# Kernel optimization log

Hardware: AMD Instinct MI355X
Metric: run time of the kernel (lower is better)

Reference implementation:

```python
import jax, jax.numpy as jnp
import numpy as np

B = 1048576
S = 8
K = 10  # n_facts
EPS = 1e-8
ENTROPY_W = 0.01
DIVERSITY_W = 0.1


def setup_inputs() -> dict:
    key = jax.random.key(0)
    k1, k2, k3, k4, k5 = jax.random.split(key, 5)
    p = jax.random.uniform(k1, (B, 2, K), dtype=jnp.float32) + 1e-3
    pCS = p / jnp.sum(p, axis=-1, keepdims=True)  # normalized probs like Categorical
    base_loss = jax.random.uniform(k2, (1,), dtype=jnp.float32)
    Y = jax.random.randint(k3, (B,), 0, 19, dtype=jnp.int32)
    samples1 = jax.random.randint(k4, (S, B), 0, K, dtype=jnp.int32)
    samples2 = jax.random.randint(k5, (S, B), 0, K, dtype=jnp.int32)
    return {"pCS": pCS, "base_loss": base_loss, "Y": Y,
            "samples1": samples1, "samples2": samples2}


def reference(pCS, base_loss, Y, samples1, samples2):
    n_facts = pCS.shape[-1]
    s = samples1.shape[0]
    p1 = pCS[:, 0, :]  # [B, K]
    p2 = pCS[:, 1, :]
    # entropy regularization
    ent1 = -jnp.sum(p1 * jnp.log(p1 + EPS), axis=-1).mean()
    ent2 = -jnp.sum(p2 * jnp.log(p2 + EPS), axis=-1).mean()
    entropy_loss = -(ent1 + ent2) / 2
    # diversity: count unique (d1,d2) pairs per batch element (vectorized bincount-style)
    pairs = (samples1 * n_facts + samples2).T  # [B, S]
    eq = pairs[:, :, None] == pairs[:, None, :]  # [B, S, S]
    earlier = jnp.tril(jnp.ones((s, s), dtype=bool), k=-1)  # j < i
    dup = jnp.any(eq & earlier[None], axis=-1)  # [B, S] True if seen before
    unique_counts = jnp.sum(~dup, axis=-1).astype(jnp.float32)  # [B]
    diversity = unique_counts.mean()
    max_diversity = min(s, n_facts * n_facts)
    diversity_ratio = diversity / max_diversity
    diversity_loss = -jnp.log(diversity_ratio + EPS)
    # REINFORCE leave-one-out (computed, not added to total in original)
    pred_labels = samples1 + samples2  # [S, B] (addition task)
    correct = (pred_labels == Y[None, :]).astype(jnp.float32)
    sample_acc = correct.mean()
    b_idx = jnp.arange(p1.shape[0])[None, :]
    log_probs = jnp.log(p1)[b_idx, samples1] + jnp.log(p2)[b_idx, samples2]  # [S, B]
    baseline = (jnp.sum(correct, axis=0, keepdims=True) - correct) / (s - 1 + EPS)
    advantage = jax.lax.stop_gradient(correct - baseline)
    rloo_loss = -jnp.mean(log_probs * advantage)
    total_loss = base_loss[0] + ENTROPY_W * entropy_loss + DIVERSITY_W * diversity_loss
    return jnp.stack([total_loss, rloo_loss, diversity_loss, sample_acc])
```

## Files before the change

kernel.cpp:

```cpp
#include <hip/hip_runtime.h>

#define S_CONST 8
#define K_CONST 10
#define EPSF 1e-8f

__global__ __launch_bounds__(256) void fml_reduce(
        const float* __restrict__ pCS,
        const int* __restrict__ Y,
        const int* __restrict__ s1g,
        const int* __restrict__ s2g,
        double* __restrict__ partials,
        int B)
{
    __shared__ float sp[4][64 * 20];
    __shared__ float red[4][4];

    const int lane = threadIdx.x & 63;
    const int wv   = threadIdx.x >> 6;
    float* sw = sp[wv];

    float ent = 0.f, uniq = 0.f, corr = 0.f, rloo = 0.f;

    const int nchunks = (B + 63) >> 6;
    const int gwaves  = gridDim.x << 2;
    for (int ch = (blockIdx.x << 2) + wv; ch < nchunks; ch += gwaves) {
        const int base = ch << 6;
        const int row  = base + lane;
        const bool full = (base + 64) <= B;
        const bool inb  = full || (row < B);

        int y = 0;
        int a1[S_CONST], a2[S_CONST];
        if (inb) {
            y = Y[row];
            #pragma unroll
            for (int s = 0; s < S_CONST; ++s) {
                a1[s] = s1g[(size_t)s * B + row];
                a2[s] = s2g[(size_t)s * B + row];
            }
        } else {
            y = -1;
            #pragma unroll
            for (int s = 0; s < S_CONST; ++s) { a1[s] = 0; a2[s] = 0; }
        }

        const float4* src = reinterpret_cast<const float4*>(pCS + (size_t)base * 20);
        float4* dst = reinterpret_cast<float4*>(sw);
        #pragma unroll
        for (int k = 0; k < 5; ++k) {
            const int g = lane + (k << 6);
            float4 v = make_float4(1.f, 1.f, 1.f, 1.f);
            if (full || (base + g / 5) < B) v = src[g];
            ent += v.x * __logf(v.x) + v.y * __logf(v.y)
                 + v.z * __logf(v.z) + v.w * __logf(v.w);
            dst[g] = v;
        }
        __builtin_amdgcn_wave_barrier();

        if (inb) {
            int pr[S_CONST];
            float c[S_CONST];
            float csum = 0.f;
            #pragma unroll
            for (int s = 0; s < S_CONST; ++s) {
                pr[s] = a1[s] * K_CONST + a2[s];
                c[s]  = (a1[s] + a2[s] == y) ? 1.f : 0.f;
                csum += c[s];
            }
            corr += csum;

            #pragma unroll
            for (int i = 0; i < S_CONST; ++i) {
                bool dup = false;
                #pragma unroll
                for (int j = 0; j < i; ++j) dup = dup || (pr[i] == pr[j]);
                uniq += dup ? 0.f : 1.f;
            }

            const float* my = &sw[lane * 20];
            #pragma unroll
            for (int s = 0; s < S_CONST; ++s) {
                const float g1 = my[a1[s]];
                const float g2 = my[10 + a2[s]];
                const float adv = c[s] - (csum - c[s]) / 7.0f;
                rloo += __logf(g1 * g2) * adv;
            }
        }
        __builtin_amdgcn_wave_barrier();
    }

    #pragma unroll
    for (int off = 32; off >= 1; off >>= 1) {
        ent  += __shfl_xor(ent,  off);
        uniq += __shfl_xor(uniq, off);
        corr += __shfl_xor(corr, off);
        rloo += __shfl_xor(rloo, off);
    }

    if (lane == 0) {
        red[wv][0] = ent; red[wv][1] = uniq;
        red[wv][2] = corr; red[wv][3] = rloo;
    }
    __syncthreads();
    if (threadIdx.x == 0) {
        double e = 0, u = 0, cs = 0, rl = 0;
        #pragma unroll
        for (int w = 0; w < 4; ++w) {
            e += (double)red[w][0]; u += (double)red[w][1];
            cs += (double)red[w][2]; rl += (double)red[w][3];
        }
        double* p = &partials[(size_t)blockIdx.x * 4];
        p[0] = e; p[1] = u; p[2] = cs; p[3] = rl;
    }
}

__global__ __launch_bounds__(1024) void fml_finalize(
        const double* __restrict__ partials,
        const float* __restrict__ base_loss,
        float* __restrict__ out, int B, int nblocks)
{
    __shared__ double red[16][4];
    double e = 0, u = 0, cs = 0, rl = 0;
    for (int i = threadIdx.x; i < nblocks; i += 1024) {
        const double* p = &partials[(size_t)i * 4];
        e += p[0]; u += p[1]; cs += p[2]; rl += p[3];
    }
    #pragma unroll
    for (int off = 32; off >= 1; off >>= 1) {
        e  += __shfl_xor(e,  off);
        u  += __shfl_xor(u,  off);
        cs += __shfl_xor(cs, off);
        rl += __shfl_xor(rl, off);
    }
    const int lane = threadIdx.x & 63;
    const int wave = threadIdx.x >> 6;
    if (lane == 0) { red[wave][0] = e; red[wave][1] = u; red[wave][2] = cs; red[wave][3] = rl; }
    __syncthreads();
    if (threadIdx.x == 0) {
        e = 0; u = 0; cs = 0; rl = 0;
        #pragma unroll
        for (int w = 0; w < 16; ++w) {
            e += red[w][0]; u += red[w][1]; cs += red[w][2]; rl += red[w][3];
        }
        const double dB = (double)B;
        const float entropy_loss = (float)(e / (2.0 * dB));
        const float diversity = (float)(u / dB);
        const float ratio = diversity / 8.0f;
        const float diversity_loss = -logf(ratio + EPSF);
        const float sample_acc = (float)(cs / (dB * (double)S_CONST));
        const float rloo_loss  = (float)(-rl / (dB * (double)S_CONST));
        out[0] = base_loss[0] + 0.01f * entropy_loss + 0.1f * diversity_loss;
        out[1] = rloo_loss;
        out[2] = diversity_loss;
        out[3] = sample_acc;
    }
}

extern "C" void kernel_launch(void* const* d_in, const int* in_sizes, int n_in,
                              void* d_out, int out_size, void* d_ws, size_t ws_size,
                              hipStream_t stream) {
    const float* pCS       = (const float*)d_in[0];
    const float* base_loss = (const float*)d_in[1];
    const int*   Y         = (const int*)d_in[2];
    const int*   s1        = (const int*)d_in[3];
    const int*   s2        = (const int*)d_in[4];
    float* out = (float*)d_out;
    const int B = in_sizes[2];

    double* partials = (double*)d_ws;

    const int block = 256;
    const int grid = 2048;
    fml_reduce<<<grid, block, 0, stream>>>(pCS, Y, s1, s2, partials, B);
    fml_finalize<<<1, 1024, 0, stream>>>(partials, base_loss, out, B, grid);
}
```

Before: 38.15 us.

## Process two chunks per wave with prefetched loads and log-table reuse

Replaces the grid-stride loop with exactly two 64-row chunks per wave. All loads for both chunks are issued up front so their memory latency overlaps. The kernel now stores log(p) in LDS instead of p, so the gathered log-probs are added rather than logged again per sample, and the advantage is computed with constant multiplies. The grid grows to cover B/128 waves (2048 blocks for this B), and each wave carries more live registers.

```diff
diff --git a/kernel.cpp b/kernel.cpp
--- a/kernel.cpp
+++ b/kernel.cpp
@@ -3,6 +3,85 @@
 #define S_CONST 8
 #define K_CONST 10
 #define EPSF 1e-8f
+
+struct Samp { int y; int a1[S_CONST]; int a2[S_CONST]; };
+
+__device__ __forceinline__ void load_samp(Samp& sm, const int* __restrict__ Y,
+                                          const int* __restrict__ s1g,
+                                          const int* __restrict__ s2g,
+                                          int B, int row, bool inb) {
+    if (inb) {
+        sm.y = Y[row];
+        #pragma unroll
+        for (int s = 0; s < S_CONST; ++s) {
+            sm.a1[s] = s1g[(size_t)s * B + row];
+            sm.a2[s] = s2g[(size_t)s * B + row];
+        }
+    } else {
+        sm.y = -1;
+        #pragma unroll
+        for (int s = 0; s < S_CONST; ++s) { sm.a1[s] = 0; sm.a2[s] = 0; }
+    }
+}
+
+__device__ __forceinline__ void load_pcs(const float* __restrict__ pCS, int base, int B,
+                                         bool full, float4 v[5], int lane) {
+    const float4* src = reinterpret_cast<const float4*>(pCS + (size_t)base * 20);
+    #pragma unroll
+    for (int k = 0; k < 5; ++k) {
+        const int g = lane + (k << 6);
+        float4 t = make_float4(1.f, 1.f, 1.f, 1.f);
+        if (full || (base + g / 5) < B) t = src[g];
+        v[k] = t;
+    }
+}
+
+__device__ __forceinline__ float ent_write(float* __restrict__ pan,
+                                           const float4 v[5], int lane) {
+    float e = 0.f;
+    float4* dst = reinterpret_cast<float4*>(pan);
+    #pragma unroll
+    for (int k = 0; k < 5; ++k) {
+        float4 lg;
+        lg.x = __logf(v[k].x); lg.y = __logf(v[k].y);
+        lg.z = __logf(v[k].z); lg.w = __logf(v[k].w);
+        e += v[k].x * lg.x + v[k].y * lg.y + v[k].z * lg.z + v[k].w * lg.w;
+        dst[lane + (k << 6)] = lg;
+    }
+    return e;
+}
+
+__device__ __forceinline__ void body(const float* __restrict__ pan, const Samp& sm,
+                                     bool inb, int lane,
+                                     float& uniq, float& corr, float& rloo) {
+    if (!inb) return;
+    int pr[S_CONST]; float c[S_CONST];
+    float csum = 0.f;
+    #pragma unroll
+    for (int s = 0; s < S_CONST; ++s) {
+        pr[s] = sm.a1[s] * K_CONST + sm.a2[s];
+        c[s]  = (sm.a1[s] + sm.a2[s] == sm.y) ? 1.f : 0.f;
+        csum += c[s];
+    }
+    corr += csum;
+
+    #pragma unroll
+    for (int i = 0; i < S_CONST; ++i) {
+        bool dup = false;
+        #pragma unroll
+        for (int j = 0; j < i; ++j) dup = dup || (pr[i] == pr[j]);
+        uniq += dup ? 0.f : 1.f;
+    }
+
+    const float* my = &pan[lane * 20];
+    const float cs7 = csum * (1.0f / 7.0f);
+    #pragma unroll
+    for (int s = 0; s < S_CONST; ++s) {
+        const float lp = my[sm.a1[s]] + my[10 + sm.a2[s]];
+        const float adv = c[s] * (8.0f / 7.0f) - cs7;
+        rloo += lp * adv;
+    }
+}
 
 __global__ __launch_bounds__(256) void fml_reduce(
         const float* __restrict__ pCS,
@@ -12,82 +91,40 @@
         double* __restrict__ partials,
         int B)
 {
-    __shared__ float sp[4][64 * 20];
+    __shared__ float lgpan[4][64 * 20];
     __shared__ float red[4][4];
 
     const int lane = threadIdx.x & 63;
     const int wv   = threadIdx.x >> 6;
-    float* sw = sp[wv];
+    float* pan = lgpan[wv];
+
+    const int nchunks = (B + 63) >> 6;
+    const int wid = (blockIdx.x << 2) + wv;
+    const int ch0 = wid * 2, ch1 = wid * 2 + 1;
+    const bool has0 = ch0 < nchunks, has1 = ch1 < nchunks;
+    const int base0 = ch0 << 6, base1 = ch1 << 6;
+    const bool full0 = has0 && (base0 + 64 <= B);
+    const bool full1 = has1 && (base1 + 64 <= B);
+    const bool inb0  = has0 && (full0 || base0 + lane < B);
+    const bool inb1  = has1 && (full1 || base1 + lane < B);
 
     float ent = 0.f, uniq = 0.f, corr = 0.f, rloo = 0.f;
-
-    const int nchunks = (B + 63) >> 6;
-    const int gwaves  = gridDim.x << 2;
-    for (int ch = (blockIdx.x << 2) + wv; ch < nchunks; ch += gwaves) {
-        const int base = ch << 6;
-        const int row  = base + lane;
-        const bool full = (base + 64) <= B;
-        const bool inb  = full || (row < B);
-
-        int y = 0;
-        int a1[S_CONST], a2[S_CONST];
-        if (inb) {
-            y = Y[row];
-            #pragma unroll
-            for (int s = 0; s < S_CONST; ++s) {
-                a1[s] = s1g[(size_t)s * B + row];
-                a2[s] = s2g[(size_t)s * B + row];
-            }
-        } else {
-            y = -1;
-            #pragma unroll
-            for (int s = 0; s < S_CONST; ++s) { a1[s] = 0; a2[s] = 0; }
-        }
-
-        const float4* src = reinterpret_cast<const float4*>(pCS + (size_t)base * 20);
-        float4* dst = reinterpret_cast<float4*>(sw);
-        #pragma unroll
-        for (int k = 0; k < 5; ++k) {
-            const int g = lane + (k << 6);
-            float4 v = make_float4(1.f, 1.f, 1.f, 1.f);
-            if (full || (base + g / 5) < B) v = src[g];
-            ent += v.x * __logf(v.x) + v.y * __logf(v.y)
-                 + v.z * __logf(v.z) + v.w * __logf(v.w);
-            dst[g] = v;
-        }
-        __builtin_amdgcn_wave_barrier();
-
-        if (inb) {
-            int pr[S_CONST];
-            float c[S_CONST];
-            float csum = 0.f;
-            #pragma unroll
-            for (int s = 0; s < S_CONST; ++s) {
-                pr[s] = a1[s] * K_CONST + a2[s];
-                c[s]  = (a1[s] + a2[s] == y) ? 1.f : 0.f;
-                csum += c[s];
-            }
-            corr += csum;
-
-            #pragma unroll
-            for (int i = 0; i < S_CONST; ++i) {
-                bool dup = false;
-                #pragma unroll
-                for (int j = 0; j < i; ++j) dup = dup || (pr[i] == pr[j]);
-                uniq += dup ? 0.f : 1.f;
-            }
-
-            const float* my = &sw[lane * 20];
-            #pragma unroll
-            for (int s = 0; s < S_CONST; ++s) {
-                const float g1 = my[a1[s]];
-                const float g2 = my[10 + a2[s]];
-                const float adv = c[s] - (csum - c[s]) / 7.0f;
-                rloo += __logf(g1 * g2) * adv;
-            }
-        }
-        __builtin_amdgcn_wave_barrier();
-    }
+    float4 v0[5], v1[5];
+    Samp sm0, sm1;
+
+    if (has0) load_pcs(pCS, base0, B, full0, v0, lane);
+    load_samp(sm0, Y, s1g, s2g, B, base0 + lane, inb0);
+    if (has1) load_pcs(pCS, base1, B, full1, v1, lane);
+
+    if (has0) ent += ent_write(pan, v0, lane);
+    load_samp(sm1, Y, s1g, s2g, B, base1 + lane, inb1);
+    __builtin_amdgcn_wave_barrier();
+    body(pan, sm0, inb0, lane, uniq, corr, rloo);
+    __builtin_amdgcn_wave_barrier();
+
+    if (has1) ent += ent_write(pan, v1, lane);
+    __builtin_amdgcn_wave_barrier();
+    body(pan, sm1, inb1, lane, uniq, corr, rloo);
 
     #pragma unroll
     for (int off = 32; off >= 1; off >>= 1) {
@@ -169,8 +206,10 @@
 
     double* partials = (double*)d_ws;
 
-    const int block = 256;
-    const int grid = 2048;
-    fml_reduce<<<grid, block, 0, stream>>>(pCS, Y, s1, s2, partials, B);
-    fml_finalize<<<1, 1024, 0, stream>>>(partials, base_loss, out, B, grid);
-}
+    const int nchunks = (B + 63) >> 6;
+    const int waves   = (nchunks + 1) >> 1;
+    const int blocks  = (waves + 3) >> 2;
+
+    fml_reduce<<<blocks, 256, 0, stream>>>(pCS, Y, s1, s2, partials, B);
+    fml_finalize<<<1, 1024, 0, stream>>>(partials, base_loss, out, B, blocks);
+}
```

Result: faster. 36.38 us (-4.6%).

## Process one row per thread in registers, replacing LDS staging and gathered logs

Applied to the files above, without the earlier changes.

Each thread now loads its own row's 20 probabilities directly as five float4 loads instead of staging a 64-row chunk through shared memory. The log of every probability is computed once and reused both for the entropy and, through predicated selects, for the REINFORCE gathers, so the 8 separate log-of-product evaluations and the dynamic LDS indexing go away. Partials are written as float4 rather than doubles. The cost is uncoalesced strided 80-byte-per-lane global loads and more register pressure from the select chains.

```diff
diff --git a/kernel.cpp b/kernel.cpp
--- a/kernel.cpp
+++ b/kernel.cpp
@@ -1,74 +1,53 @@
 #include <hip/hip_runtime.h>
 
 #define S_CONST 8
-#define K_CONST 10
 #define EPSF 1e-8f
 
-__global__ __launch_bounds__(256) void fml_reduce(
+__device__ __forceinline__ void elem(int j, float p, const int a[S_CONST],
+                                     float g[S_CONST], float& ent) {
+    const float lg = __logf(p);
+    ent += p * lg;
+    #pragma unroll
+    for (int s = 0; s < S_CONST; ++s) g[s] = (a[s] == j) ? lg : g[s];
+}
+
+__global__ __launch_bounds__(256) void fml_rows(
         const float* __restrict__ pCS,
         const int* __restrict__ Y,
         const int* __restrict__ s1g,
         const int* __restrict__ s2g,
-        double* __restrict__ partials,
+        float4* __restrict__ partials,
         int B)
 {
-    __shared__ float sp[4][64 * 20];
-    __shared__ float red[4][4];
-
-    const int lane = threadIdx.x & 63;
-    const int wv   = threadIdx.x >> 6;
-    float* sw = sp[wv];
-
     float ent = 0.f, uniq = 0.f, corr = 0.f, rloo = 0.f;
 
-    const int nchunks = (B + 63) >> 6;
-    const int gwaves  = gridDim.x << 2;
-    for (int ch = (blockIdx.x << 2) + wv; ch < nchunks; ch += gwaves) {
-        const int base = ch << 6;
-        const int row  = base + lane;
-        const bool full = (base + 64) <= B;
-        const bool inb  = full || (row < B);
+    const int gid = blockIdx.x * 256 + threadIdx.x;
+    const int gstride = gridDim.x * 256;
 
-        int y = 0;
+    #pragma unroll 1
+    for (int row = gid; row < B; row += gstride) {
+        const float4* rp = reinterpret_cast<const float4*>(pCS + (size_t)row * 20);
+        const float4 v0 = rp[0], v1 = rp[1], v2 = rp[2], v3 = rp[3], v4 = rp[4];
+        const int y = Y[row];
         int a1[S_CONST], a2[S_CONST];
-        if (inb) {
-            y = Y[row];
-            #pragma unroll
-            for (int s = 0; s < S_CONST; ++s) {
-                a1[s] = s1g[(size_t)s * B + row];
-                a2[s] = s2g[(size_t)s * B + row];
-            }
-        } else {
-            y = -1;
-            #pragma unroll
-            for (int s = 0; s < S_CONST; ++s) { a1[s] = 0; a2[s] = 0; }
+        #pragma unroll
+        for (int s = 0; s < S_CONST; ++s) {
+            a1[s] = s1g[(size_t)s * B + row];
+            a2[s] = s2g[(size_t)s * B + row];
         }
 
-        const float4* src = reinterpret_cast<const float4*>(pCS + (size_t)base * 20);
-        float4* dst = reinterpret_cast<float4*>(sw);
+        float c[S_CONST], csum = 0.f;
         #pragma unroll
-        for (int k = 0; k < 5; ++k) {
-            const int g = lane + (k << 6);
-            float4 v = make_float4(1.f, 1.f, 1.f, 1.f);
-            if (full || (base + g / 5) < B) v = src[g];
-            ent += v.x * __logf(v.x) + v.y * __logf(v.y)
-                 + v.z * __logf(v.z) + v.w * __logf(v.w);
-            dst[g] = v;
+        for (int s = 0; s < S_CONST; ++s) {
+            c[s] = (a1[s] + a2[s] == y) ? 1.f : 0.f;
+            csum += c[s];
         }
-        __builtin_amdgcn_wave_barrier();
+        corr += csum;
 
-        if (inb) {
+        {
             int pr[S_CONST];
-            float c[S_CONST];
-            float csum = 0.f;
             #pragma unroll
-            for (int s = 0; s < S_CONST; ++s) {
-                pr[s] = a1[s] * K_CONST + a2[s];
-                c[s]  = (a1[s] + a2[s] == y) ? 1.f : 0.f;
-                csum += c[s];
-            }
-            corr += csum;
-
+            for (int s = 0; s < S_CONST; ++s) pr[s] = a1[s] * 10 + a2[s];
             #pragma unroll
             for (int i = 0; i < S_CONST; ++i) {
                 bool dup = false;
@@ -76,17 +55,34 @@
                 for (int j = 0; j < i; ++j) dup = dup || (pr[i] == pr[j]);
                 uniq += dup ? 0.f : 1.f;
             }
+        }
 
-            const float* my = &sw[lane * 20];
-            #pragma unroll
-            for (int s = 0; s < S_CONST; ++s) {
-                const float g1 = my[a1[s]];
-                const float g2 = my[10 + a2[s]];
-                const float adv = c[s] - (csum - c[s]) / 7.0f;
-                rloo += __logf(g1 * g2) * adv;
-            }
-        }
-        __builtin_amdgcn_wave_barrier();
+        float adv[S_CONST];
+        #pragma unroll
+        for (int s = 0; s < S_CONST; ++s)
+            adv[s] = c[s] * (8.0f / 7.0f) - csum * (1.0f / 7.0f);
+
+        float g1[S_CONST];
+        #pragma unroll
+        for (int s = 0; s < S_CONST; ++s) g1[s] = 0.f;
+        elem(0, v0.x, a1, g1, ent); elem(1, v0.y, a1, g1, ent);
+        elem(2, v0.z, a1, g1, ent); elem(3, v0.w, a1, g1, ent);
+        elem(4, v1.x, a1, g1, ent); elem(5, v1.y, a1, g1, ent);
+        elem(6, v1.z, a1, g1, ent); elem(7, v1.w, a1, g1, ent);
+        elem(8, v2.x, a1, g1, ent); elem(9, v2.y, a1, g1, ent);
+        #pragma unroll
+        for (int s = 0; s < S_CONST; ++s) rloo += g1[s] * adv[s];
+
+        float g2[S_CONST];
+        #pragma unroll
+        for (int s = 0; s < S_CONST; ++s) g2[s] = 0.f;
+        elem(0, v2.z, a2, g2, ent); elem(1, v2.w, a2, g2, ent);
+        elem(2, v3.x, a2, g2, ent); elem(3, v3.y, a2, g2, ent);
+        elem(4, v3.z, a2, g2, ent); elem(5, v3.w, a2, g2, ent);
+        elem(6, v4.x, a2, g2, ent); elem(7, v4.y, a2, g2, ent);
+        elem(8, v4.z, a2, g2, ent); elem(9, v4.w, a2, g2, ent);
+        #pragma unroll
+        for (int s = 0; s < S_CONST; ++s) rloo += g2[s] * adv[s];
     }
 
     #pragma unroll
@@ -97,33 +93,34 @@
         rloo += __shfl_xor(rloo, off);
     }
 
+    __shared__ float red[4][4];
+    const int lane = threadIdx.x & 63;
+    const int wv   = threadIdx.x >> 6;
     if (lane == 0) {
         red[wv][0] = ent; red[wv][1] = uniq;
         red[wv][2] = corr; red[wv][3] = rloo;
     }
     __syncthreads();
     if (threadIdx.x == 0) {
-        double e = 0, u = 0, cs = 0, rl = 0;
-        #pragma unroll
-        for (int w = 0; w < 4; ++w) {
-            e += (double)red[w][0]; u += (double)red[w][1];
-            cs += (double)red[w][2]; rl += (double)red[w][3];
-        }
-        double* p = &partials[(size_t)blockIdx.x * 4];
-        p[0] = e; p[1] = u; p[2] = cs; p[3] = rl;
+        float4 p;
+        p.x = red[0][0] + red[1][0] + red[2][0] + red[3][0];
+        p.y = red[0][1] + red[1][1] + red[2][1] + red[3][1];
+        p.z = red[0][2] + red[1][2] + red[2][2] + red[3][2];
+        p.w = red[0][3] + red[1][3] + red[2][3] + red[3][3];
+        partials[blockIdx.x] = p;
     }
 }
 
 __global__ __launch_bounds__(1024) void fml_finalize(
-        const double* __restrict__ partials,
+        const float4* __restrict__ partials,
         const float* __restrict__ base_loss,
         float* __restrict__ out, int B, int nblocks)
 {
     __shared__ double red[16][4];
     double e = 0, u = 0, cs = 0, rl = 0;
     for (int i = threadIdx.x; i < nblocks; i += 1024) {
-        const double* p = &partials[(size_t)i * 4];
-        e += p[0]; u += p[1]; cs += p[2]; rl += p[3];
+        const float4 p = partials[i];
+        e += (double)p.x; u += (double)p.y; cs += (double)p.z; rl += (double)p.w;
     }
     #pragma unroll
     for (int off = 32; off >= 1; off >>= 1) {
@@ -167,10 +164,9 @@
     float* out = (float*)d_out;
     const int B = in_sizes[2];
 
-    double* partials = (double*)d_ws;
+    float4* partials = (float4*)d_ws;
 
-    const int block = 256;
     const int grid = 2048;
-    fml_reduce<<<grid, block, 0, stream>>>(pCS, Y, s1, s2, partials, B);
+    fml_rows<<<grid, 256, 0, stream>>>(pCS, Y, s1, s2, partials, B);
     fml_finalize<<<1, 1024, 0, stream>>>(partials, base_loss, out, B, grid);
 }
```

After: 42.21 us. 10.7% more time.
